# Kernel tuning notes

Hardware: AMD Instinct MI355X
Metric: run time of the kernel (lower is better)

## Reference

```python
import jax, jax.numpy as jnp
import numpy as np

B, S, HID = 1, 2048, 2048
H, HKV, D = 16, 4, 128
GROUPS = H // HKV
SCALE = D ** -0.5


def rotate_half(x):
    x1, x2 = x[..., : x.shape[-1] // 2], x[..., x.shape[-1] // 2 :]
    return jnp.concatenate((-x2, x1), axis=-1)


def setup_inputs() -> dict:
    key = jax.random.key(0)
    ks = jax.random.split(key, 8)
    hidden_states = jax.random.normal(ks[0], (B, S, HID), dtype=jnp.float32)
    # standard RoPE tables, base 10000
    inv_freq = 1.0 / (10000.0 ** (np.arange(0, D, 2, dtype=np.float32) / D))
    t = np.arange(S, dtype=np.float32)
    freqs = np.outer(t, inv_freq)                      # (S, D/2)
    emb = np.concatenate([freqs, freqs], axis=-1)      # (S, D)
    cos = jnp.asarray(np.cos(emb)[None], dtype=jnp.float32)  # (1, S, D)
    sin = jnp.asarray(np.sin(emb)[None], dtype=jnp.float32)
    std = 0.02
    Wq = jax.random.normal(ks[1], (HID, H * D), dtype=jnp.float32) * std
    Wk = jax.random.normal(ks[2], (HID, HKV * D), dtype=jnp.float32) * std
    Wv = jax.random.normal(ks[3], (HID, HKV * D), dtype=jnp.float32) * std
    Wg = jax.random.normal(ks[4], (HID, HKV), dtype=jnp.float32) * std
    Wo = jax.random.normal(ks[5], (H * D, HID), dtype=jnp.float32) * std
    return {"hidden_states": hidden_states, "cos": cos, "sin": sin,
            "Wq": Wq, "Wk": Wk, "Wv": Wv, "Wg": Wg, "Wo": Wo}


def reference(hidden_states, cos, sin, Wq, Wk, Wv, Wg, Wo):
    b, s, _ = hidden_states.shape
    # projections -> (B, heads, S, D)
    q = (hidden_states @ Wq).reshape(b, s, H, D).transpose(0, 2, 1, 3)
    k = (hidden_states @ Wk).reshape(b, s, HKV, D).transpose(0, 2, 1, 3)
    v = (hidden_states @ Wv).reshape(b, s, HKV, D).transpose(0, 2, 1, 3)
    g = (hidden_states @ Wg).transpose(0, 2, 1)                 # (B, HKV, S)
    g = jax.nn.log_sigmoid(g.astype(jnp.float32))
    # RoPE
    c, sn = cos[:, None, :, :], sin[:, None, :, :]
    q = q * c + rotate_half(q) * sn
    k = k * c + rotate_half(k) * sn
    # GQA repeat kv heads
    k = jnp.repeat(k, GROUPS, axis=1)
    v = jnp.repeat(v, GROUPS, axis=1)
    g = jnp.repeat(g, GROUPS, axis=1)                           # (B, H, S)
    # gated power retention, deg=2, parallel (quadratic) form
    G = jnp.cumsum(g, axis=-1)                                  # (B, H, S)
    # decay_ij = exp(G_i - G_j) for j <= i  (<= 1 since logsigmoid < 0)
    logdecay = G[..., :, None] - G[..., None, :]                # (B, H, S, S)
    causal = jnp.tril(jnp.ones((s, s), dtype=bool))
    decay = jnp.where(causal, jnp.exp(logdecay), 0.0)
    qk = jnp.einsum("bhid,bhjd->bhij", q, k) * SCALE
    scores = (qk * qk) * decay                                  # deg=2 power scores
    den = jnp.maximum(jnp.sum(scores, axis=-1, keepdims=True), 1.0)
    out = jnp.einsum("bhij,bhjd->bhid", scores, v) / den        # (B, H, S, D)
    out = out.transpose(0, 2, 1, 3).reshape(b, s, H * D)
    return out @ Wo
```

## Files before the change

### kernel.cpp

```cpp
#include <hip/hip_runtime.h>
#include <hip/hip_bf16.h>

#define S_LEN 2048
#define HID   2048
#define NH    16
#define NKV   4
#define HD    128
#define KVD   512
#define NQKV  3072
#define SCALE2 0.0078125f
#define NCH   80

typedef __bf16 bf16;
typedef __attribute__((ext_vector_type(8))) __bf16 bf16x8;
typedef __attribute__((ext_vector_type(4))) __bf16 bf16x4;
typedef __attribute__((ext_vector_type(4))) float f32x4;

__device__ __forceinline__ void gload_lds16(const bf16* g, bf16* l) {
    __builtin_amdgcn_global_load_lds((const __attribute__((address_space(1))) void*)g,
                                     (__attribute__((address_space(3))) void*)l, 16, 0, 0);
}

__device__ __forceinline__ void transpose_tile(const float* __restrict__ W,
                                               bf16* __restrict__ Wt,
                                               int K, int N, int bx, int by,
                                               int t, float (*Ts)[65])
{
    const int kb = bx * 64, nb = by * 64;
    const int tr = t >> 6, tc = t & 63;
    #pragma unroll
    for (int p = 0; p < 16; ++p) {
        int k = p * 4 + tr;
        Ts[k][tc] = W[(size_t)(kb + k) * N + nb + tc];
    }
    __syncthreads();
    const int nr = t >> 3, kc = t & 7;
    #pragma unroll
    for (int p = 0; p < 2; ++p) {
        int n = p * 32 + nr;
        bf16x8 o;
        #pragma unroll
        for (int x = 0; x < 8; ++x) o[x] = (bf16)Ts[kc * 8 + x][n];
        *(bf16x8*)&Wt[(size_t)(nb + n) * K + kb + kc * 8] = o;
    }
}

__global__ __launch_bounds__(256) void prep_kernel(const float* __restrict__ hs,
                                                   const float* __restrict__ Wq,
                                                   const float* __restrict__ Wk,
                                                   const float* __restrict__ Wv,
                                                   const float* __restrict__ Wo,
                                                   const float* __restrict__ Wg,
                                                   bf16* __restrict__ hsb,
                                                   bf16* __restrict__ WcatT,
                                                   bf16* __restrict__ WoT,
                                                   float* __restrict__ graw,
                                                   float* __restrict__ outz)
{
    __shared__ float Ts[64][65];
    __shared__ float red[4][4];
    const int b = blockIdx.x, tid = threadIdx.x;

    if (b < 2048) {
        int i = (b * 256 + tid) * 8;
        const float4* qp = (const float4*)&hs[i];
        float4 a = qp[0], c = qp[1];
        bf16x8 r;
        r[0]=(bf16)a.x; r[1]=(bf16)a.y; r[2]=(bf16)a.z; r[3]=(bf16)a.w;
        r[4]=(bf16)c.x; r[5]=(bf16)c.y; r[6]=(bf16)c.z; r[7]=(bf16)c.w;
        *(bf16x8*)&hsb[i] = r;

        const float4* wgp = (const float4*)&Wg[tid * 32];
        float h[8] = {a.x, a.y, a.z, a.w, c.x, c.y, c.z, c.w};
        float a0 = 0.f, a1 = 0.f, a2 = 0.f, a3 = 0.f;
        #pragma unroll
        for (int x = 0; x < 8; ++x) {
            float4 w = wgp[x];
            a0 += h[x] * w.x; a1 += h[x] * w.y;
            a2 += h[x] * w.z; a3 += h[x] * w.w;
        }
        #pragma unroll
        for (int off = 32; off >= 1; off >>= 1) {
            a0 += __shfl_xor(a0, off); a1 += __shfl_xor(a1, off);
            a2 += __shfl_xor(a2, off); a3 += __shfl_xor(a3, off);
        }
        const int w4 = tid >> 6;
        if ((tid & 63) == 0) {
            red[w4][0] = a0; red[w4][1] = a1; red[w4][2] = a2; red[w4][3] = a3;
        }
        __syncthreads();
        if (tid == 0) {
            #pragma unroll
            for (int cc = 0; cc < 4; ++cc) {
                float x = red[0][cc] + red[1][cc] + red[2][cc] + red[3][cc];
                graw[cc * S_LEN + b] = fminf(x, 0.f) - log1pf(expf(-fabsf(x)));
            }
        }
    } else if (b < 3072) {
        int lb = b - 2048;
        transpose_tile(Wq, WcatT, HID, HID, lb >> 5, lb & 31, tid, Ts);
    } else if (b < 3328) {
        int lb = b - 3072;
        transpose_tile(Wk, WcatT + (size_t)2048 * HID, HID, KVD, lb >> 3, lb & 7, tid, Ts);
    } else if (b < 3584) {
        int lb = b - 3328;
        transpose_tile(Wv, WcatT + (size_t)2560 * HID, HID, KVD, lb >> 3, lb & 7, tid, Ts);
    } else if (b < 4608) {
        int lb = b - 3584;
        transpose_tile(Wo, WoT, HID, HID, lb >> 5, lb & 31, tid, Ts);
    } else {
        int i = ((b - 4608) * 256 + tid) * 8;
        float4 z = make_float4(0.f, 0.f, 0.f, 0.f);
        *(float4*)&outz[i] = z;
        *(float4*)&outz[i + 4] = z;
    }
}

__device__ __forceinline__ void gemm128_core(const bf16* __restrict__ A,
                                             const bf16* __restrict__ Bt,
                                             int K, int k0, int k1, int mb, int nb,
                                             bf16 (*As)[32], bf16 (*Bs)[32],
                                             f32x4 (*acc)[4],
                                             int w, int l16, int quad, int lane)
{
    const int m0 = (w & 1) * 64, n0 = (w >> 1) * 64;
    const int srow = lane >> 2, scol = (lane & 3) * 8;

    for (int kt = k0; kt < k1; kt += 32) {
        __syncthreads();
        gload_lds16(&A [(size_t)(mb + w * 32 +      srow) * K + kt + scol], &As[w * 32     ][0]);
        gload_lds16(&A [(size_t)(mb + w * 32 + 16 + srow) * K + kt + scol], &As[w * 32 + 16][0]);
        gload_lds16(&Bt[(size_t)(nb + w * 32 +      srow) * K + kt + scol], &Bs[w * 32     ][0]);
        gload_lds16(&Bt[(size_t)(nb + w * 32 + 16 + srow) * K + kt + scol], &Bs[w * 32 + 16][0]);
        __syncthreads();

        bf16x8 af[4], bfr[4];
        #pragma unroll
        for (int t = 0; t < 4; ++t) af[t]  = *(const bf16x8*)&As[m0 + t * 16 + l16][quad * 8];
        #pragma unroll
        for (int u = 0; u < 4; ++u) bfr[u] = *(const bf16x8*)&Bs[n0 + u * 16 + l16][quad * 8];
        #pragma unroll
        for (int t = 0; t < 4; ++t)
            #pragma unroll
            for (int u = 0; u < 4; ++u)
                acc[t][u] = __builtin_amdgcn_mfma_f32_16x16x32_bf16(af[t], bfr[u], acc[t][u], 0, 0, 0);
    }
}

__device__ __forceinline__ void gemm128_bk64(const bf16* __restrict__ A,
                                             const bf16* __restrict__ Bt,
                                             int K, int k0, int k1, int mb, int nb,
                                             bf16 (*As)[64], bf16 (*Bs)[64],
                                             f32x4 (*acc)[4],
                                             int w, int l16, int quad, int lane)
{
    const int m0 = (w & 1) * 64, n0 = (w >> 1) * 64;
    const int srow8 = lane >> 3;
    const int scol8 = ((lane & 7) ^ srow8) * 8;
    const bf16* aP[4]; const bf16* bP[4];
    #pragma unroll
    for (int i = 0; i < 4; ++i) {
        aP[i] = &A [(size_t)(mb + w * 32 + i * 8 + srow8) * K + k0 + scol8];
        bP[i] = &Bt[(size_t)(nb + w * 32 + i * 8 + srow8) * K + k0 + scol8];
    }
    const int rsw = (l16 & 7) << 3;

    const int nk = k1 - k0;
    for (int kt = 0; kt < nk; kt += 64) {
        __syncthreads();
        #pragma unroll
        for (int i = 0; i < 4; ++i) {
            gload_lds16(aP[i] + kt, &As[w * 32 + i * 8][0]);
            gload_lds16(bP[i] + kt, &Bs[w * 32 + i * 8][0]);
        }
        __syncthreads();

        #pragma unroll
        for (int kk = 0; kk < 2; ++kk) {
            bf16x8 af[4], bfr[4];
            #pragma unroll
            for (int t = 0; t < 4; ++t)
                af[t]  = *(const bf16x8*)&As[m0 + t * 16 + l16][(kk * 32 + quad * 8) ^ rsw];
            #pragma unroll
            for (int u = 0; u < 4; ++u)
                bfr[u] = *(const bf16x8*)&Bs[n0 + u * 16 + l16][(kk * 32 + quad * 8) ^ rsw];
            #pragma unroll
            for (int t = 0; t < 4; ++t)
                #pragma unroll
                for (int u = 0; u < 4; ++u)
                    acc[t][u] = __builtin_amdgcn_mfma_f32_16x16x32_bf16(af[t], bfr[u], acc[t][u], 0, 0, 0);
        }
    }
}

__global__ __launch_bounds__(256) void gemm_qkv_kernel(const bf16* __restrict__ A,
                                                       const bf16* __restrict__ Wt,
                                                       float* __restrict__ qsl,
                                                       float* __restrict__ ksl,
                                                       float* __restrict__ vsl,
                                                       int M, int K)
{
    __shared__ __attribute__((aligned(16))) bf16 As[128][32];
    __shared__ __attribute__((aligned(16))) bf16 Bs[128][32];
    const int tid = threadIdx.x, w = tid >> 6, lane = tid & 63;
    const int l16 = lane & 15, quad = lane >> 4;

    const int bid = blockIdx.x;
    const int lin = (bid & 7) * 48 + (bid >> 3);
    const int mb = (lin / 24) * 128, nb = (lin % 24) * 128;

    const int m0 = (w & 1) * 64, n0 = (w >> 1) * 64;
    const int z = blockIdx.z, kh = K >> 1, k0 = z * kh;

    float* qd = qsl + (size_t)z * S_LEN * HID;
    float* kd = ksl + (size_t)z * S_LEN * KVD;
    float* vd = vsl + (size_t)z * S_LEN * KVD;

    f32x4 acc[4][4] = {};
    gemm128_core(A, Wt, K, k0, k0 + kh, mb, nb, As, Bs, acc, w, l16, quad, lane);

    #pragma unroll
    for (int t = 0; t < 4; ++t)
        #pragma unroll
        for (int u = 0; u < 4; ++u)
            #pragma unroll
            for (int r = 0; r < 4; ++r) {
                int row = mb + m0 + t * 16 + quad * 4 + r;
                int col = nb + n0 + u * 16 + l16;
                float val = acc[t][u][r];
                if (nb < 2048)       qd[(size_t)row * HID + col] = val;
                else if (nb < 2560)  kd[(size_t)row * KVD + (col - 2048)] = val;
                else                 vd[(size_t)(col - 2560) * S_LEN + row] = val;
            }
}

__global__ __launch_bounds__(256) void gemm_wo_kernel(const bf16* __restrict__ A,
                                                      const bf16* __restrict__ Bt,
                                                      float* __restrict__ C,
                                                      int M, int N, int K)
{
    __shared__ __attribute__((aligned(16))) bf16 As[128][64];
    __shared__ __attribute__((aligned(16))) bf16 Bs[128][64];
    const int tid = threadIdx.x, w = tid >> 6, lane = tid & 63;
    const int l16 = lane & 15, quad = lane >> 4;

    const int bid = blockIdx.x;
    const int lin = (bid & 7) * 32 + (bid >> 3);
    const int mb = (lin >> 4) * 128, nb = (lin & 15) * 128;

    const int m0 = (w & 1) * 64, n0 = (w >> 1) * 64;
    const int kh = K >> 1, k0 = blockIdx.z * kh;

    f32x4 acc[4][4] = {};
    gemm128_bk64(A, Bt, K, k0, k0 + kh, mb, nb, As, Bs, acc, w, l16, quad, lane);

    #pragma unroll
    for (int t = 0; t < 4; ++t)
        #pragma unroll
        for (int u = 0; u < 4; ++u)
            #pragma unroll
            for (int r = 0; r < 4; ++r) {
                int row = mb + m0 + t * 16 + quad * 4 + r;
                int col = nb + n0 + u * 16 + l16;
                unsafeAtomicAdd(&C[(size_t)row * N + col], acc[t][u][r]);
            }
}

#define RQB2 2048
#define RKB2 512
#define RVB  512
__global__ __launch_bounds__(256) void rope_kernel(const float* __restrict__ qsl,
                                                   const float* __restrict__ ksl,
                                                   const float* __restrict__ vsl,
                                                   bf16* __restrict__ qb,
                                                   bf16* __restrict__ kb,
                                                   bf16* __restrict__ vT,
                                                   const float* __restrict__ cosb,
                                                   const float* __restrict__ sinb,
                                                   const float* __restrict__ graw,
                                                   float* __restrict__ G)
{
    const int blk = blockIdx.x;
    if (blk < RQB2 + RKB2) {
        int idx;
        const float* src; size_t ssz; bf16* dst; int s, rem, stride;
        if (blk < RQB2) {
            idx = (blk * 256 + threadIdx.x) * 4;
            src = qsl; ssz = (size_t)S_LEN * HID; dst = qb; stride = HID;
            s = idx / (NH * 64); rem = idx % (NH * 64);
        } else {
            idx = ((blk - RQB2) * 256 + threadIdx.x) * 4;
            src = ksl; ssz = (size_t)S_LEN * KVD; dst = kb; stride = KVD;
            s = idx / (NKV * 64); rem = idx % (NKV * 64);
        }
        int h = rem >> 6, d = rem & 63;
        size_t base = (size_t)s * stride + h * 128 + d;
        float4 lo0 = *(const float4*)&src[base];
        float4 lo1 = *(const float4*)&src[ssz + base];
        float4 hi0 = *(const float4*)&src[base + 64];
        float4 hi1 = *(const float4*)&src[ssz + base + 64];
        float4 cl  = *(const float4*)&cosb[s * 128 + d];
        float4 ch  = *(const float4*)&cosb[s * 128 + d + 64];
        float4 sl  = *(const float4*)&sinb[s * 128 + d];
        float4 sh  = *(const float4*)&sinb[s * 128 + d + 64];
        float x0[4] = {lo0.x + lo1.x, lo0.y + lo1.y, lo0.z + lo1.z, lo0.w + lo1.w};
        float x1[4] = {hi0.x + hi1.x, hi0.y + hi1.y, hi0.z + hi1.z, hi0.w + hi1.w};
        float clo[4] = {cl.x, cl.y, cl.z, cl.w}, chi[4] = {ch.x, ch.y, ch.z, ch.w};
        float slo[4] = {sl.x, sl.y, sl.z, sl.w}, shi[4] = {sh.x, sh.y, sh.z, sh.w};
        bf16x4 olo, ohi;
        #pragma unroll
        for (int x = 0; x < 4; ++x) {
            olo[x] = (bf16)(x0[x] * clo[x] - x1[x] * slo[x]);
            ohi[x] = (bf16)(x1[x] * chi[x] + x0[x] * shi[x]);
        }
        *(bf16x4*)&dst[base]      = olo;
        *(bf16x4*)&dst[base + 64] = ohi;
    } else if (blk < RQB2 + RKB2 + RVB) {
        int i = ((blk - RQB2 - RKB2) * 256 + threadIdx.x) * 8;
        const size_t ssz = (size_t)S_LEN * KVD;
        float4 u0 = *(const float4*)&vsl[i],       u1 = *(const float4*)&vsl[i + 4];
        float4 v0 = *(const float4*)&vsl[ssz + i], v1 = *(const float4*)&vsl[ssz + i + 4];
        bf16x8 r;
        r[0] = (bf16)(u0.x + v0.x); r[1] = (bf16)(u0.y + v0.y);
        r[2] = (bf16)(u0.z + v0.z); r[3] = (bf16)(u0.w + v0.w);
        r[4] = (bf16)(u1.x + v1.x); r[5] = (bf16)(u1.y + v1.y);
        r[6] = (bf16)(u1.z + v1.z); r[7] = (bf16)(u1.w + v1.w);
        *(bf16x8*)&vT[i] = r;
    } else {
        const int c = blk - (RQB2 + RKB2 + RVB);
        const int t = threadIdx.x;
        __shared__ float sums[256];
        float loc[8];
        float run = 0.f;
        #pragma unroll
        for (int i = 0; i < 8; ++i) { run += graw[c * S_LEN + t * 8 + i]; loc[i] = run; }
        sums[t] = run;
        __syncthreads();
        for (int off = 1; off < 256; off <<= 1) {
            float add = (t >= off) ? sums[t - off] : 0.f;
            __syncthreads();
            sums[t] += add;
            __syncthreads();
        }
        float offset = sums[t] - run;
        #pragma unroll
        for (int i = 0; i < 8; ++i) G[c * S_LEN + t * 8 + i] = offset + loc[i];
    }
}

__global__ __launch_bounds__(256) void attn_kernel(const bf16* __restrict__ q,
                                                   const bf16* __restrict__ k,
                                                   const bf16* __restrict__ vT,
                                                   const float* __restrict__ G,
                                                   bf16* __restrict__ out,
                                                   float* __restrict__ pO,
                                                   float* __restrict__ pden)
{
    int rem = blockIdx.x, qt = 0, cch = 0;
    #pragma unroll
    for (int g = 0; g < 4; ++g) {
        int sz = 8 * (g + 1);
        if (rem < sz) { qt = g * 8 + rem / (g + 1); cch = rem % (g + 1); break; }
        rem -= sz;
    }
    const int gg = qt >> 3, nc = gg + 1;
    const int jt0 = cch * 8, jt1 = min(qt + 1, jt0 + 8);

    const int h = blockIdx.y, kvh = h >> 2;
    const int qb = qt * 64;
    const int tid = threadIdx.x, w = tid >> 6, lane = tid & 63;
    const int l16 = lane & 15, quad = lane >> 4;

    __shared__ __attribute__((aligned(16))) bf16 Ks4[4][64][32];
    __shared__ __attribute__((aligned(16))) bf16 Vt4[2][128][32];
    __shared__ __attribute__((aligned(16))) bf16 Sb[4][16][68];

    bf16x8 qf[4];
    const int qrow = qb + w * 16 + l16;
    #pragma unroll
    for (int kc = 0; kc < 4; ++kc)
        qf[kc] = *(const bf16x8*)&q[(size_t)qrow * HID + h * HD + kc * 32 + quad * 8];

    const int irow = qb + w * 16 + quad * 4;
    float Gq[4];
    #pragma unroll
    for (int r = 0; r < 4; ++r) Gq[r] = G[kvh * S_LEN + irow + r];

    const int sr4 = lane >> 2, sc4 = (lane & 3) * 8;
    const int vkk = w >> 1, vdg = (w & 1) * 4;

    f32x4 acco[8] = {};
    float den[4] = {0.f, 0.f, 0.f, 0.f};

    for (int kt = jt0; kt < jt1; ++kt) {
        const int jb = kt * 64;
        __syncthreads();
        #pragma unroll
        for (int rg = 0; rg < 4; ++rg)
            gload_lds16(&k[(size_t)(jb + rg * 16 + sr4) * KVD + kvh * HD + w * 32 + sc4],
                        &Ks4[w][rg * 16][0]);
        #pragma unroll
        for (int it = 0; it < 4; ++it)
            gload_lds16(&vT[(size_t)(kvh * HD + (vdg + it) * 16 + sr4) * S_LEN + jb + vkk * 32 + sc4],
                        &Vt4[vkk][(vdg + it) * 16][0]);
        __syncthreads();

        f32x4 accs[4] = {};
        #pragma unroll
        for (int t = 0; t < 4; ++t)
            #pragma unroll
            for (int kc = 0; kc < 4; ++kc) {
                bf16x8 bfr = *(const bf16x8*)&Ks4[kc][t * 16 + l16][quad * 8];
                accs[t] = __builtin_amdgcn_mfma_f32_16x16x32_bf16(qf[kc], bfr, accs[t], 0, 0, 0);
            }

        const float Gt = G[kvh * S_LEN + jb];
        float sr[4];
        #pragma unroll
        for (int r = 0; r < 4; ++r) sr[r] = SCALE2 * __expf(Gq[r] - Gt);
        #pragma unroll
        for (int t = 0; t < 4; ++t) {
            int j = jb + t * 16 + l16;
            float colF = __expf(fminf(Gt - G[kvh * S_LEN + j], 85.f));
            #pragma unroll
            for (int r = 0; r < 4; ++r) {
                float d0 = accs[t][r];
                float sc = (j <= irow + r) ? d0 * d0 * sr[r] * colF : 0.f;
                den[r] += sc;
                Sb[w][quad * 4 + r][t * 16 + l16] = (bf16)sc;
            }
        }

        #pragma unroll
        for (int kk = 0; kk < 2; ++kk) {
            bf16x8 af = *(const bf16x8*)&Sb[w][l16][kk * 32 + quad * 8];
            #pragma unroll
            for (int dt = 0; dt < 8; ++dt) {
                bf16x8 bfr = *(const bf16x8*)&Vt4[kk][dt * 16 + l16][quad * 8];
                acco[dt] = __builtin_amdgcn_mfma_f32_16x16x32_bf16(af, bfr, acco[dt], 0, 0, 0);
            }
        }
    }

    #pragma unroll
    for (int r = 0; r < 4; ++r) {
        #pragma unroll
        for (int off = 1; off < 16; off <<= 1) den[r] += __shfl_xor(den[r], off);
    }

    if (nc == 1) {
        float dinv[4];
        #pragma unroll
        for (int r = 0; r < 4; ++r) dinv[r] = 1.f / fmaxf(den[r], 1.f);
        #pragma unroll
        for (int dt = 0; dt < 8; ++dt)
            #pragma unroll
            for (int r = 0; r < 4; ++r)
                out[(size_t)(irow + r) * HID + h * HD + dt * 16 + l16] =
                    (bf16)(acco[dt][r] * dinv[r]);
    } else {
        const int slot = h * NCH + 4 * gg * (gg + 1) + (qt & 7) * (gg + 1) + cch;
        float* po = &pO[(size_t)slot * 8192];
        const int lr = w * 16 + quad * 4;
        #pragma unroll
        for (int dt = 0; dt < 8; ++dt)
            #pragma unroll
            for (int r = 0; r < 4; ++r)
                po[(lr + r) * 128 + dt * 16 + l16] = acco[dt][r];
        if (l16 == 0) {
            #pragma unroll
            for (int r = 0; r < 4; ++r) pden[slot * 64 + lr + r] = den[r];
        }
    }
}

__global__ __launch_bounds__(256) void attn_reduce_kernel(const float* __restrict__ pO,
                                                          const float* __restrict__ pden,
                                                          bf16* __restrict__ out)
{
    const int p = blockIdx.x;
    const int h = p / 24, qt = 8 + p % 24;
    const int gg = qt >> 3, nc = gg + 1;
    const int base = h * NCH + 4 * gg * (gg + 1) + (qt & 7) * (gg + 1);
    const int qb = qt * 64;
    const int tid = threadIdx.x;

    __shared__ float sden[64];
    if (tid < 64) {
        float s = 0.f;
        for (int c = 0; c < nc; ++c) s += pden[(base + c) * 64 + tid];
        sden[tid] = 1.f / fmaxf(s, 1.f);
    }
    __syncthreads();

    #pragma unroll
    for (int i = 0; i < 8; ++i) {
        int e = i * 1024 + tid * 4;
        float4 s = make_float4(0.f, 0.f, 0.f, 0.f);
        for (int c = 0; c < nc; ++c) {
            float4 v = *(const float4*)&pO[(size_t)(base + c) * 8192 + e];
            s.x += v.x; s.y += v.y; s.z += v.z; s.w += v.w;
        }
        int lr = e >> 7, col = e & 127;
        float di = sden[lr];
        bf16* o = &out[(size_t)(qb + lr) * HID + h * HD + col];
        o[0] = (bf16)(s.x * di); o[1] = (bf16)(s.y * di);
        o[2] = (bf16)(s.z * di); o[3] = (bf16)(s.w * di);
    }
}

extern "C" void kernel_launch(void* const* d_in, const int* in_sizes, int n_in,
                              void* d_out, int out_size, void* d_ws, size_t ws_size,
                              hipStream_t stream)
{
    const float* hs   = (const float*)d_in[0];
    const float* cosb = (const float*)d_in[1];
    const float* sinb = (const float*)d_in[2];
    const float* Wq   = (const float*)d_in[3];
    const float* Wk   = (const float*)d_in[4];
    const float* Wv   = (const float*)d_in[5];
    const float* Wg   = (const float*)d_in[6];
    const float* Wo   = (const float*)d_in[7];
    float* out = (float*)d_out;

    char* p = (char*)d_ws;
    bf16*  qbuf  = (bf16*)p;  p += (size_t)S_LEN * HID * 2;
    bf16*  kbuf  = (bf16*)p;  p += (size_t)S_LEN * KVD * 2;
    bf16*  vT    = (bf16*)p;  p += (size_t)S_LEN * KVD * 2;
    bf16*  abuf  = (bf16*)p;  p += (size_t)S_LEN * HID * 2;
    bf16*  hsb   = (bf16*)p;  p += (size_t)S_LEN * HID * 2;
    bf16*  WcatT = (bf16*)p;  p += (size_t)NQKV * HID * 2;
    bf16*  WoT   = (bf16*)p;  p += (size_t)HID * HID * 2;
    float* graw  = (float*)p; p += (size_t)NKV * S_LEN * 4;
    float* G     = (float*)p; p += (size_t)NKV * S_LEN * 4;
    float* pO    = (float*)p; p += (size_t)NH * NCH * 8192 * 4;
    float* pden  = (float*)p; p += (size_t)NH * NCH * 64 * 4;

    float* qsl = pO;
    float* ksl = pO + (size_t)8 * 1024 * 1024;
    float* vsl = (float*)abuf;

    prep_kernel<<<6656, 256, 0, stream>>>(hs, Wq, Wk, Wv, Wo, Wg,
                                          hsb, WcatT, WoT, graw, out);
    gemm_qkv_kernel<<<dim3(384, 1, 2), 256, 0, stream>>>(hsb, WcatT, qsl, ksl, vsl, S_LEN, HID);
    rope_kernel<<<RQB2 + RKB2 + RVB + NKV, 256, 0, stream>>>(qsl, ksl, vsl, qbuf, kbuf, vT,
                                                             cosb, sinb, graw, G);
    attn_kernel<<<dim3(NCH, NH), 256, 0, stream>>>(qbuf, kbuf, vT, G, abuf, pO, pden);
    attn_reduce_kernel<<<NH * 24, 256, 0, stream>>>(pO, pden, abuf);
    gemm_wo_kernel<<<dim3(256, 1, 2), 256, 0, stream>>>(abuf, WoT, out, S_LEN, HID, HID);
}
```

Before: 275.5 us.

## Enlarge attention query tile to 128 rows per block for K/V reuse

Each attention block now handles 128 query rows (two 16-row MFMA sub-tiles per wave) instead of 64, so every K/V tile loaded into LDS feeds twice as many MFMAs. The chunk scheduling, partial-output slots and the reduce kernel are re-indexed for 128-row tiles. This halves K/V global traffic and block count, at the cost of more registers per thread and fewer blocks (640), which may reduce occupancy and load balance.

```diff
diff --git a/kernel.cpp b/kernel.cpp
--- a/kernel.cpp
+++ b/kernel.cpp
@@ -10,6 +10,7 @@
 #define NQKV  3072
 #define SCALE2 0.0078125f
 #define NCH   80
+#define NCH2  40
 
 typedef __bf16 bf16;
 typedef __attribute__((ext_vector_type(8))) __bf16 bf16x8;
@@ -359,38 +360,44 @@
     int rem = blockIdx.x, qt = 0, cch = 0;
     #pragma unroll
     for (int g = 0; g < 4; ++g) {
-        int sz = 8 * (g + 1);
-        if (rem < sz) { qt = g * 8 + rem / (g + 1); cch = rem % (g + 1); break; }
+        int sz = 4 * (g + 1);
+        if (rem < sz) { qt = g * 4 + rem / (g + 1); cch = rem % (g + 1); break; }
         rem -= sz;
     }
-    const int gg = qt >> 3, nc = gg + 1;
-    const int jt0 = cch * 8, jt1 = min(qt + 1, jt0 + 8);
+    const int gg = qt >> 2, nc = gg + 1;
+    const int jt0 = cch * 8, jt1 = min(2 * qt + 2, jt0 + 8);
 
     const int h = blockIdx.y, kvh = h >> 2;
-    const int qb = qt * 64;
+    const int qb = qt * 128;
     const int tid = threadIdx.x, w = tid >> 6, lane = tid & 63;
     const int l16 = lane & 15, quad = lane >> 4;
 
     __shared__ __attribute__((aligned(16))) bf16 Ks4[4][64][32];
     __shared__ __attribute__((aligned(16))) bf16 Vt4[2][128][32];
-    __shared__ __attribute__((aligned(16))) bf16 Sb[4][16][68];
-
-    bf16x8 qf[4];
-    const int qrow = qb + w * 16 + l16;
-    #pragma unroll
-    for (int kc = 0; kc < 4; ++kc)
-        qf[kc] = *(const bf16x8*)&q[(size_t)qrow * HID + h * HD + kc * 32 + quad * 8];
-
-    const int irow = qb + w * 16 + quad * 4;
-    float Gq[4];
-    #pragma unroll
-    for (int r = 0; r < 4; ++r) Gq[r] = G[kvh * S_LEN + irow + r];
+    __shared__ __attribute__((aligned(16))) bf16 Sb[4][32][68];
+
+    bf16x8 qf[2][4];
+    #pragma unroll
+    for (int qh = 0; qh < 2; ++qh) {
+        const int qrow = qb + w * 32 + qh * 16 + l16;
+        #pragma unroll
+        for (int kc = 0; kc < 4; ++kc)
+            qf[qh][kc] = *(const bf16x8*)&q[(size_t)qrow * HID + h * HD + kc * 32 + quad * 8];
+    }
+
+    const int irow0 = qb + w * 32 + quad * 4;
+    float Gq[2][4];
+    #pragma unroll
+    for (int qh = 0; qh < 2; ++qh)
+        #pragma unroll
+        for (int r = 0; r < 4; ++r)
+            Gq[qh][r] = G[kvh * S_LEN + irow0 + qh * 16 + r];
 
     const int sr4 = lane >> 2, sc4 = (lane & 3) * 8;
     const int vkk = w >> 1, vdg = (w & 1) * 4;
 
-    f32x4 acco[8] = {};
-    float den[4] = {0.f, 0.f, 0.f, 0.f};
+    f32x4 acco[2][8] = {};
+    float den[2][4] = {};
 
     for (int kt = jt0; kt < jt1; ++kt) {
         const int jb = kt * 64;
@@ -405,71 +412,91 @@
                         &Vt4[vkk][(vdg + it) * 16][0]);
         __syncthreads();
 
-        f32x4 accs[4] = {};
+        f32x4 accs[2][4] = {};
         #pragma unroll
         for (int t = 0; t < 4; ++t)
             #pragma unroll
             for (int kc = 0; kc < 4; ++kc) {
                 bf16x8 bfr = *(const bf16x8*)&Ks4[kc][t * 16 + l16][quad * 8];
-                accs[t] = __builtin_amdgcn_mfma_f32_16x16x32_bf16(qf[kc], bfr, accs[t], 0, 0, 0);
+                accs[0][t] = __builtin_amdgcn_mfma_f32_16x16x32_bf16(qf[0][kc], bfr, accs[0][t], 0, 0, 0);
+                accs[1][t] = __builtin_amdgcn_mfma_f32_16x16x32_bf16(qf[1][kc], bfr, accs[1][t], 0, 0, 0);
             }
 
         const float Gt = G[kvh * S_LEN + jb];
-        float sr[4];
-        #pragma unroll
-        for (int r = 0; r < 4; ++r) sr[r] = SCALE2 * __expf(Gq[r] - Gt);
+        float sr[2][4];
+        #pragma unroll
+        for (int qh = 0; qh < 2; ++qh)
+            #pragma unroll
+            for (int r = 0; r < 4; ++r)
+                sr[qh][r] = SCALE2 * __expf(Gq[qh][r] - Gt);
         #pragma unroll
         for (int t = 0; t < 4; ++t) {
             int j = jb + t * 16 + l16;
             float colF = __expf(fminf(Gt - G[kvh * S_LEN + j], 85.f));
             #pragma unroll
-            for (int r = 0; r < 4; ++r) {
-                float d0 = accs[t][r];
-                float sc = (j <= irow + r) ? d0 * d0 * sr[r] * colF : 0.f;
-                den[r] += sc;
-                Sb[w][quad * 4 + r][t * 16 + l16] = (bf16)sc;
-            }
+            for (int qh = 0; qh < 2; ++qh)
+                #pragma unroll
+                for (int r = 0; r < 4; ++r) {
+                    float d0 = accs[qh][t][r];
+                    float sc = (j <= irow0 + qh * 16 + r) ? d0 * d0 * sr[qh][r] * colF : 0.f;
+                    den[qh][r] += sc;
+                    Sb[w][qh * 16 + quad * 4 + r][t * 16 + l16] = (bf16)sc;
+                }
         }
 
         #pragma unroll
         for (int kk = 0; kk < 2; ++kk) {
-            bf16x8 af = *(const bf16x8*)&Sb[w][l16][kk * 32 + quad * 8];
+            bf16x8 af0 = *(const bf16x8*)&Sb[w][l16     ][kk * 32 + quad * 8];
+            bf16x8 af1 = *(const bf16x8*)&Sb[w][16 + l16][kk * 32 + quad * 8];
             #pragma unroll
             for (int dt = 0; dt < 8; ++dt) {
                 bf16x8 bfr = *(const bf16x8*)&Vt4[kk][dt * 16 + l16][quad * 8];
-                acco[dt] = __builtin_amdgcn_mfma_f32_16x16x32_bf16(af, bfr, acco[dt], 0, 0, 0);
+                acco[0][dt] = __builtin_amdgcn_mfma_f32_16x16x32_bf16(af0, bfr, acco[0][dt], 0, 0, 0);
+                acco[1][dt] = __builtin_amdgcn_mfma_f32_16x16x32_bf16(af1, bfr, acco[1][dt], 0, 0, 0);
             }
         }
     }
 
     #pragma unroll
-    for (int r = 0; r < 4; ++r) {
-        #pragma unroll
-        for (int off = 1; off < 16; off <<= 1) den[r] += __shfl_xor(den[r], off);
-    }
+    for (int qh = 0; qh < 2; ++qh)
+        #pragma unroll
+        for (int r = 0; r < 4; ++r) {
+            #pragma unroll
+            for (int off = 1; off < 16; off <<= 1)
+                den[qh][r] += __shfl_xor(den[qh][r], off);
+        }
 
     if (nc == 1) {
-        float dinv[4];
-        #pragma unroll
-        for (int r = 0; r < 4; ++r) dinv[r] = 1.f / fmaxf(den[r], 1.f);
+        float dinv[2][4];
+        #pragma unroll
+        for (int qh = 0; qh < 2; ++qh)
+            #pragma unroll
+            for (int r = 0; r < 4; ++r) dinv[qh][r] = 1.f / fmaxf(den[qh][r], 1.f);
         #pragma unroll
         for (int dt = 0; dt < 8; ++dt)
             #pragma unroll
-            for (int r = 0; r < 4; ++r)
-                out[(size_t)(irow + r) * HID + h * HD + dt * 16 + l16] =
-                    (bf16)(acco[dt][r] * dinv[r]);
+            for (int qh = 0; qh < 2; ++qh)
+                #pragma unroll
+                for (int r = 0; r < 4; ++r)
+                    out[(size_t)(irow0 + qh * 16 + r) * HID + h * HD + dt * 16 + l16] =
+                        (bf16)(acco[qh][dt][r] * dinv[qh][r]);
     } else {
-        const int slot = h * NCH + 4 * gg * (gg + 1) + (qt & 7) * (gg + 1) + cch;
-        float* po = &pO[(size_t)slot * 8192];
-        const int lr = w * 16 + quad * 4;
+        const int slot = h * NCH2 + 2 * gg * (gg + 1) + (qt & 3) * (gg + 1) + cch;
+        float* po = &pO[(size_t)slot * 16384];
+        const int lr0 = w * 32 + quad * 4;
         #pragma unroll
         for (int dt = 0; dt < 8; ++dt)
             #pragma unroll
-            for (int r = 0; r < 4; ++r)
-                po[(lr + r) * 128 + dt * 16 + l16] = acco[dt][r];
+            for (int qh = 0; qh < 2; ++qh)
+                #pragma unroll
+                for (int r = 0; r < 4; ++r)
+                    po[(lr0 + qh * 16 + r) * 128 + dt * 16 + l16] = acco[qh][dt][r];
         if (l16 == 0) {
             #pragma unroll
-            for (int r = 0; r < 4; ++r) pden[slot * 64 + lr + r] = den[r];
+            for (int qh = 0; qh < 2; ++qh)
+                #pragma unroll
+                for (int r = 0; r < 4; ++r)
+                    pden[slot * 128 + lr0 + qh * 16 + r] = den[qh][r];
         }
     }
 }
@@ -479,26 +506,26 @@
                                                           bf16* __restrict__ out)
 {
     const int p = blockIdx.x;
-    const int h = p / 24, qt = 8 + p % 24;
-    const int gg = qt >> 3, nc = gg + 1;
-    const int base = h * NCH + 4 * gg * (gg + 1) + (qt & 7) * (gg + 1);
-    const int qb = qt * 64;
+    const int h = p / 12, qt = 4 + p % 12;
+    const int gg = qt >> 2, nc = gg + 1;
+    const int base = h * NCH2 + 2 * gg * (gg + 1) + (qt & 3) * (gg + 1);
+    const int qb = qt * 128;
     const int tid = threadIdx.x;
 
-    __shared__ float sden[64];
-    if (tid < 64) {
+    __shared__ float sden[128];
+    if (tid < 128) {
         float s = 0.f;
-        for (int c = 0; c < nc; ++c) s += pden[(base + c) * 64 + tid];
+        for (int c = 0; c < nc; ++c) s += pden[(base + c) * 128 + tid];
         sden[tid] = 1.f / fmaxf(s, 1.f);
     }
     __syncthreads();
 
     #pragma unroll
-    for (int i = 0; i < 8; ++i) {
+    for (int i = 0; i < 16; ++i) {
         int e = i * 1024 + tid * 4;
         float4 s = make_float4(0.f, 0.f, 0.f, 0.f);
         for (int c = 0; c < nc; ++c) {
-            float4 v = *(const float4*)&pO[(size_t)(base + c) * 8192 + e];
+            float4 v = *(const float4*)&pO[(size_t)(base + c) * 16384 + e];
             s.x += v.x; s.y += v.y; s.z += v.z; s.w += v.w;
         }
         int lr = e >> 7, col = e & 127;
@@ -545,7 +572,7 @@
     gemm_qkv_kernel<<<dim3(384, 1, 2), 256, 0, stream>>>(hsb, WcatT, qsl, ksl, vsl, S_LEN, HID);
     rope_kernel<<<RQB2 + RKB2 + RVB + NKV, 256, 0, stream>>>(qsl, ksl, vsl, qbuf, kbuf, vT,
                                                              cosb, sinb, graw, G);
-    attn_kernel<<<dim3(NCH, NH), 256, 0, stream>>>(qbuf, kbuf, vT, G, abuf, pO, pden);
-    attn_reduce_kernel<<<NH * 24, 256, 0, stream>>>(pO, pden, abuf);
+    attn_kernel<<<dim3(NCH2, NH), 256, 0, stream>>>(qbuf, kbuf, vT, G, abuf, pO, pden);
+    attn_reduce_kernel<<<NH * 12, 256, 0, stream>>>(pO, pden, abuf);
     gemm_wo_kernel<<<dim3(256, 1, 2), 256, 0, stream>>>(abuf, WoT, out, S_LEN, HID, HID);
 }
```

Measured after the change: 301.5 us. 9.5% more time.
